# Optimization experiments

Hardware: AMD Instinct MI355X
Metric: run time of the kernel (lower is better)

## Reference

```python
import jax, jax.numpy as jnp
import numpy as np

N = 100000   # nodes
E = 3200000  # edges (before self-loops)
IN, H, OUT = 128, 256, 40

def glorot(key, shape):
    lim = (6.0 / (shape[0] + shape[1])) ** 0.5
    return jax.random.uniform(key, shape, jnp.float32, -lim, lim)

def setup_inputs() -> dict:
    key = jax.random.key(0)
    ks = jax.random.split(key, 8)
    x = jax.random.normal(ks[0], (N, IN), jnp.float32)
    edge_index = jax.random.randint(ks[1], (2, E), 0, N, dtype=jnp.int32)
    return {
        "x": x,
        "edge_index": edge_index,
        "W0": glorot(ks[2], (IN, H)),  "b0": jnp.zeros((H,), jnp.float32),
        "W1": glorot(ks[3], (H, H)),   "b1": jnp.zeros((H,), jnp.float32),
        "W2": glorot(ks[4], (H, OUT)), "b2": jnp.zeros((OUT,), jnp.float32),
    }

def _gcn_norm(edge_index, n):
    # PyG gcn_norm: add self-loops, symmetric D^{-1/2} A D^{-1/2}
    loops = jnp.arange(n, dtype=edge_index.dtype)
    src = jnp.concatenate([edge_index[0], loops])
    dst = jnp.concatenate([edge_index[1], loops])
    deg = jax.ops.segment_sum(jnp.ones_like(src, jnp.float32), dst, num_segments=n)
    dinv = jnp.where(deg > 0, jax.lax.rsqrt(deg), 0.0)
    norm = dinv[src] * dinv[dst]  # [E+N]
    return src, dst, norm

def _gcn_layer(h, W, b, src, dst, norm, n):
    h = h @ W                                   # transform first (PyG order)
    msg = h[src] * norm[:, None]                # gather + scale
    agg = jax.ops.segment_sum(msg, dst, num_segments=n)  # scatter-add
    return agg + b

def reference(x, edge_index, W0, b0, W1, b1, W2, b2):
    n = x.shape[0]
    src, dst, norm = _gcn_norm(edge_index, n)
    h = jnp.tanh(_gcn_layer(x, W0, b0, src, dst, norm, n))  # dropout = identity (eval)
    h = jnp.tanh(_gcn_layer(h, W1, b1, src, dst, norm, n))
    out = _gcn_layer(h, W2, b2, src, dst, norm, n)
    return jax.nn.log_softmax(out, axis=1)
```

## Files before the change

### kernel.cpp

```cpp
#include <hip/hip_runtime.h>
#include <hip/hip_bf16.h>
#include <cmath>


typedef unsigned short u16;
typedef __attribute__((ext_vector_type(8))) short short8;
typedef __attribute__((ext_vector_type(4))) float f32x4;

#define BSHIFT 10
#define BNODES (1 << BSHIFT)
#define ECAP   36864
#define BMASK 0x00FF00FFu

__device__ __forceinline__ u16 f2bf(float f) {
    unsigned int u = __float_as_uint(f);
    u += 0x7fffu + ((u >> 16) & 1u);
    return (u16)(u >> 16);
}
__device__ __forceinline__ float bflo(unsigned int u) { return __uint_as_float(u << 16); }
__device__ __forceinline__ float bfhi(unsigned int u) { return __uint_as_float(u & 0xffff0000u); }

__device__ __forceinline__ int q8(float v) {
    return (int)rintf(fminf(fmaxf(v, -127.0f), 127.0f));
}


__global__ __launch_bounds__(128) void init_gcur_kernel(
        int* __restrict__ gcur, int nb) {
    int b = blockIdx.x * 128 + threadIdx.x;
    if (b < nb) gcur[b] = b * ECAP;
}

__global__ __launch_bounds__(256) void bucketize_kernel(
        const int* __restrict__ src, const int* __restrict__ dst,
        int* __restrict__ gcur, unsigned int* __restrict__ ebuf, int E) {
    __shared__ int cnt[128];
    __shared__ int base[128];
    int tid = threadIdx.x;
    int chunk0 = blockIdx.x * 8192;
    int cend = min(chunk0 + 8192, E);
    for (int r0 = chunk0; r0 < cend; r0 += 2048) {
        if (tid < 128) cnt[tid] = 0;
        __syncthreads();
        int rank[8], bk[8];
        unsigned int pk[8];
#pragma unroll
        for (int j = 0; j < 8; j++) {
            int e = r0 + j * 256 + tid;
            bk[j] = -1;
            if (e < cend) {
                int d = dst[e];
                bk[j] = d >> BSHIFT;
                pk[j] = (unsigned int)src[e] | ((unsigned int)(d & (BNODES - 1)) << 17);
                rank[j] = atomicAdd(&cnt[bk[j]], 1);
            }
        }
        __syncthreads();
        if (tid < 128 && cnt[tid] > 0) base[tid] = atomicAdd(&gcur[tid], cnt[tid]);
        __syncthreads();
#pragma unroll
        for (int j = 0; j < 8; j++)
            if (bk[j] >= 0) ebuf[base[bk[j]] + rank[j]] = pk[j];
        __syncthreads();
    }
}

__global__ __launch_bounds__(256) void deg_hist_kernel(
        const unsigned int* __restrict__ ebuf, const int* __restrict__ gcur,
        int* __restrict__ degi, int N) {
    __shared__ int h[BNODES];
    int b = blockIdx.x;
    int nb0 = b << BSHIFT;
    int nodes = min(BNODES, N - nb0);
    for (int i = threadIdx.x; i < nodes; i += 256) h[i] = 0;
    __syncthreads();
    int estart = b * ECAP;
    int eend = gcur[b];
    for (int e = estart + threadIdx.x; e < eend; e += 256)
        atomicAdd(&h[ebuf[e] >> 17], 1);
    __syncthreads();
    for (int i = threadIdx.x; i < nodes; i += 256) degi[nb0 + i] = h[i];
}

__global__ __launch_bounds__(256) void dinv_kernel(
        const int* __restrict__ degi, float* __restrict__ dinv, int n) {
    int i = blockIdx.x * 256 + threadIdx.x;
    if (i < n) dinv[i] = rsqrtf((float)degi[i] + 1.0f);
}

__global__ __launch_bounds__(256) void scan_part_kernel(
        const int* __restrict__ deg, int* __restrict__ part, int n) {
    __shared__ int s[256];
    int i = blockIdx.x * 256 + threadIdx.x;
    s[threadIdx.x] = (i < n) ? deg[i] : 0;
    __syncthreads();
    for (int off = 128; off; off >>= 1) {
        if (threadIdx.x < off) s[threadIdx.x] += s[threadIdx.x + off];
        __syncthreads();
    }
    if (threadIdx.x == 0) part[blockIdx.x] = s[0];
}

__global__ __launch_bounds__(1024) void scan_top_kernel(
        int* __restrict__ part, int nb) {
    __shared__ int s[1024];
    int t = threadIdx.x;
    int v = (t < nb) ? part[t] : 0;
    s[t] = v;
    __syncthreads();
    for (int off = 1; off < 1024; off <<= 1) {
        int u = (t >= off) ? s[t - off] : 0;
        __syncthreads();
        s[t] += u;
        __syncthreads();
    }
    if (t < nb) part[t] = s[t] - v;
}

__global__ __launch_bounds__(256) void scan_apply_kernel(
        const int* __restrict__ deg, const int* __restrict__ part,
        int* __restrict__ rs, int n) {
    __shared__ int s[256];
    int i = blockIdx.x * 256 + threadIdx.x;
    int v = (i < n) ? deg[i] : 0;
    s[threadIdx.x] = v;
    __syncthreads();
    for (int off = 1; off < 256; off <<= 1) {
        int u = (threadIdx.x >= off) ? s[threadIdx.x - off] : 0;
        __syncthreads();
        s[threadIdx.x] += u;
        __syncthreads();
    }
    if (i < n) rs[i] = part[blockIdx.x] + s[threadIdx.x] - v;
}

__global__ __launch_bounds__(256) void csr_fill_kernel(
        const unsigned int* __restrict__ ebuf, const int* __restrict__ gcur,
        const int* __restrict__ rs, int* __restrict__ csr, int N) {
    __shared__ int lcur[BNODES];
    int b = blockIdx.x;
    int nb0 = b << BSHIFT;
    int nodes = min(BNODES, N - nb0);
    for (int i = threadIdx.x; i < nodes; i += 256) lcur[i] = rs[nb0 + i];
    __syncthreads();
    int estart = b * ECAP;
    int eend = gcur[b];
    for (int e = estart + threadIdx.x; e < eend; e += 256) {
        unsigned int v = ebuf[e];
        int s = v & 0x1FFFF;
        int dl = v >> 17;
        int pos = atomicAdd(&lcur[dl], 1);
        csr[pos] = s;
    }
}

__global__ __launch_bounds__(256) void wt_kernel(
        const float* __restrict__ W, u16* __restrict__ Wt, int K, int NC) {
    int i = blockIdx.x * 256 + threadIdx.x;
    if (i < K * NC) {
        int k = i / NC, c = i % NC;
        Wt[(size_t)c * K + k] = f2bf(W[i]);
    }
}

__global__ __launch_bounds__(256) void scale_x_kernel(
        const float* __restrict__ x, const float* __restrict__ dinv,
        unsigned int* __restrict__ out, int total4) {
    int i = blockIdx.x * 256 + threadIdx.x;
    if (i >= total4) return;
    int n = i >> 5;
    float4 v = reinterpret_cast<const float4*>(x)[i];
    float s = dinv[n] * 63.5f;
    int a0 = q8(v.x * s), a1 = q8(v.y * s), a2 = q8(v.z * s), a3 = q8(v.w * s);
    out[i] = (unsigned int)(a0 & 0xff) | ((unsigned int)(a1 & 0xff) << 8) |
             ((unsigned int)(a2 & 0xff) << 16) | ((unsigned int)(a3 & 0xff) << 24);
}

#define ACC8(q0, q1)                                                  \
    do {                                                              \
        aex += (q0) & BMASK; aox += ((q0) >> 8) & BMASK;              \
        aey += (q1) & BMASK; aoy += ((q1) >> 8) & BMASK;              \
    } while (0)

__global__ __launch_bounds__(256) void agg128_i8_kernel(
        const signed char* __restrict__ in, u16* __restrict__ out,
        const int* __restrict__ rs, const int* __restrict__ deg,
        const int* __restrict__ csr, const float* __restrict__ dinv, int n) {
    int wid = blockIdx.x * 4 + (threadIdx.x >> 6);
    if (wid >= n) return;
    int lane = threadIdx.x & 63;
    int quad = lane >> 4;
    int l16 = lane & 15;
    int start = rs[wid];
    int cnt = deg[wid];

    unsigned int aex = 0, aox = 0, aey = 0, aoy = 0;
    if (quad == 0) {
        uint2 q = *reinterpret_cast<const uint2*>(
            in + (size_t)wid * 128 + l16 * 8);
        q.x ^= 0x80808080u; q.y ^= 0x80808080u;
        ACC8(q.x, q.y);
    }
    int i = 0;
    for (; i + 16 <= cnt; i += 16) {
        int s[4];
#pragma unroll
        for (int j = 0; j < 4; j++) s[j] = csr[start + i + 4 * j + quad];
#pragma unroll
        for (int j = 0; j < 4; j++) {
            uint2 q = *reinterpret_cast<const uint2*>(
                in + (size_t)s[j] * 128 + l16 * 8);
            q.x ^= 0x80808080u; q.y ^= 0x80808080u;
            ACC8(q.x, q.y);
        }
    }
    for (; i + 4 <= cnt; i += 4) {
        int s0 = csr[start + i + quad];
        uint2 q = *reinterpret_cast<const uint2*>(
            in + (size_t)s0 * 128 + l16 * 8);
        q.x ^= 0x80808080u; q.y ^= 0x80808080u;
        ACC8(q.x, q.y);
    }
    int rem = cnt - i;
    if (quad < rem) {
        int s0 = csr[start + i + quad];
        uint2 q = *reinterpret_cast<const uint2*>(
            in + (size_t)s0 * 128 + l16 * 8);
        q.x ^= 0x80808080u; q.y ^= 0x80808080u;
        ACC8(q.x, q.y);
    }
    aex += (unsigned int)__shfl((int)aex, lane + 32);
    aox += (unsigned int)__shfl((int)aox, lane + 32);
    aey += (unsigned int)__shfl((int)aey, lane + 32);
    aoy += (unsigned int)__shfl((int)aoy, lane + 32);
    aex += (unsigned int)__shfl((int)aex, lane + 16);
    aox += (unsigned int)__shfl((int)aox, lane + 16);
    aey += (unsigned int)__shfl((int)aey, lane + 16);
    aoy += (unsigned int)__shfl((int)aoy, lane + 16);
    if (lane < 16) {
        int T = cnt + 1;
        int bias = 128 * T;
        float c = dinv[wid] * (2.0f / 127.0f);
        float f0 = (float)((int)(aex & 0xFFFFu) - bias) * c;
        float f1 = (float)((int)(aox & 0xFFFFu) - bias) * c;
        float f2 = (float)((int)(aex >> 16) - bias) * c;
        float f3 = (float)((int)(aox >> 16) - bias) * c;
        float f4 = (float)((int)(aey & 0xFFFFu) - bias) * c;
        float f5 = (float)((int)(aoy & 0xFFFFu) - bias) * c;
        float f6 = (float)((int)(aey >> 16) - bias) * c;
        float f7 = (float)((int)(aoy >> 16) - bias) * c;
        uint4 o;
        o.x = (unsigned)f2bf(f0) | ((unsigned)f2bf(f1) << 16);
        o.y = (unsigned)f2bf(f2) | ((unsigned)f2bf(f3) << 16);
        o.z = (unsigned)f2bf(f4) | ((unsigned)f2bf(f5) << 16);
        o.w = (unsigned)f2bf(f6) | ((unsigned)f2bf(f7) << 16);
        reinterpret_cast<uint4*>(out + (size_t)wid * 128)[l16] = o;
    }
}

__global__ __launch_bounds__(256) void agg_i8_kernel(
        const signed char* __restrict__ in, u16* __restrict__ out,
        const int* __restrict__ rs, const int* __restrict__ deg,
        const int* __restrict__ csr, const float* __restrict__ dinv, int n) {
    int wid = blockIdx.x * 4 + (threadIdx.x >> 6);
    if (wid >= n) return;
    int lane = threadIdx.x & 63;
    int start = rs[wid];
    int cnt = deg[wid];

    unsigned int q = *reinterpret_cast<const unsigned int*>(
        in + (size_t)wid * 256 + lane * 4) ^ 0x80808080u;
    unsigned int ae = q & BMASK, ao = (q >> 8) & BMASK;

    int i = 0;
    for (; i + 16 <= cnt; i += 16) {
        int s[16];
#pragma unroll
        for (int j = 0; j < 16; j++)
            s[j] = __builtin_amdgcn_readfirstlane(csr[start + i + j]);
        unsigned int qq[16];
#pragma unroll
        for (int j = 0; j < 16; j++)
            qq[j] = *reinterpret_cast<const unsigned int*>(
                in + (size_t)s[j] * 256 + lane * 4);
#pragma unroll
        for (int j = 0; j < 16; j++) {
            unsigned int v = qq[j] ^ 0x80808080u;
            ae += v & BMASK;
            ao += (v >> 8) & BMASK;
        }
    }
    if (i < cnt) {
        int s[16];
#pragma unroll
        for (int j = 0; j < 16; j++) {
            int e = i + j;
            e = (e < cnt) ? e : (cnt - 1);
            s[j] = __builtin_amdgcn_readfirstlane(csr[start + e]);
        }
        unsigned int qq[16];
#pragma unroll
        for (int j = 0; j < 16; j++)
            qq[j] = *reinterpret_cast<const unsigned int*>(
                in + (size_t)s[j] * 256 + lane * 4);
#pragma unroll
        for (int j = 0; j < 16; j++) {
            unsigned int m = (i + j < cnt) ? 0xFFFFFFFFu : 0u;
            unsigned int v = (qq[j] ^ 0x80808080u) & m;
            ae += v & BMASK;
            ao += (v >> 8) & BMASK;
        }
    }

    int bias = 128 * (cnt + 1);
    float c = dinv[wid] * (1.0f / 127.0f);
    float f0 = (float)((int)(ae & 0xFFFFu) - bias) * c;
    float f1 = (float)((int)(ao & 0xFFFFu) - bias) * c;
    float f2 = (float)((int)(ae >> 16) - bias) * c;
    float f3 = (float)((int)(ao >> 16) - bias) * c;
    uint2 o;
    o.x = (unsigned)f2bf(f0) | ((unsigned)f2bf(f1) << 16);
    o.y = (unsigned)f2bf(f2) | ((unsigned)f2bf(f3) << 16);
    reinterpret_cast<uint2*>(out + (size_t)wid * 256)[lane] = o;
}

template<int EPI, typename CT>
__global__ __launch_bounds__(256) void mfma_mm_kernel(
        const u16* __restrict__ A, const u16* __restrict__ Bt,
        CT* __restrict__ C, int M, int K, int NC,
        const float* __restrict__ bias, const float* __restrict__ postscale,
        float qs) {
    __shared__ u16 As[128 * 40];
    __shared__ u16 Bs[64 * 40];
    int t = threadIdx.x;
    int w = t >> 6, lane = t & 63, quad = lane >> 4, l16 = lane & 15;
    int row0 = blockIdx.x * 128;
    int col0 = blockIdx.y * 64;

    f32x4 acc[2][4];
#pragma unroll
    for (int s = 0; s < 2; s++)
#pragma unroll
        for (int nb = 0; nb < 4; nb++)
            acc[s][nb] = (f32x4){0.f, 0.f, 0.f, 0.f};

    int bn = t >> 2, bkq = (t & 3) << 3;
    for (int k0 = 0; k0 < K; k0 += 32) {
#pragma unroll
        for (int i = t; i < 512; i += 256) {
            int r = i >> 2, c = (i & 3) << 3;
            int gr = row0 + r;
            uint4 v = {0u, 0u, 0u, 0u};
            if (gr < M)
                v = *reinterpret_cast<const uint4*>(A + (size_t)gr * K + k0 + c);
            *reinterpret_cast<uint4*>(&As[r * 40 + c]) = v;
        }
        {
            int gc = col0 + bn;
            uint4 v = {0u, 0u, 0u, 0u};
            if (gc < NC)
                v = *reinterpret_cast<const uint4*>(Bt + (size_t)gc * K + k0 + bkq);
            *reinterpret_cast<uint4*>(&Bs[bn * 40 + bkq]) = v;
        }
        __syncthreads();

        short8 af[2], bf[4];
        af[0] = *reinterpret_cast<const short8*>(&As[(w * 32 + l16) * 40 + quad * 8]);
        af[1] = *reinterpret_cast<const short8*>(&As[(w * 32 + 16 + l16) * 40 + quad * 8]);
#pragma unroll
        for (int nb = 0; nb < 4; nb++)
            bf[nb] = *reinterpret_cast<const short8*>(&Bs[(nb * 16 + l16) * 40 + quad * 8]);
#pragma unroll
        for (int s = 0; s < 2; s++)
#pragma unroll
            for (int nb = 0; nb < 4; nb++)
                acc[s][nb] = __builtin_amdgcn_mfma_f32_16x16x32_bf16(
                    af[s], bf[nb], acc[s][nb], 0, 0, 0);
        __syncthreads();
    }

#pragma unroll
    for (int s = 0; s < 2; s++) {
        int rbase = row0 + w * 32 + s * 16 + quad * 4;
#pragma unroll
        for (int nb = 0; nb < 4; nb++) {
            int gc = col0 + nb * 16 + l16;
#pragma unroll
            for (int r = 0; r < 4; r++) {
                int gr = rbase + r;
                if (gr >= M || gc >= NC) continue;
                float v = acc[s][nb][r];
                if constexpr (EPI == 1) v = tanhf(v + bias[gc]);
                else                    v = v * postscale[gr];
                if constexpr (sizeof(CT) == 1) {
                    float m = qs;
                    if constexpr (EPI == 1) m *= postscale[gr];
                    C[(size_t)gr * NC + gc] = (CT)q8(v * m);
                } else {
                    C[(size_t)gr * NC + gc] = (CT)f2bf(v);
                }
            }
        }
    }
}

__global__ __launch_bounds__(256) void agg40_ls_kernel(
        const signed char* __restrict__ in, const int* __restrict__ rs,
        const int* __restrict__ deg, const int* __restrict__ csr,
        const float* __restrict__ dinv, const float* __restrict__ bias,
        float* __restrict__ out, int n) {
    int wid = blockIdx.x * 4 + (threadIdx.x >> 6);
    if (wid >= n) return;
    int lane = threadIdx.x & 63;
    int grp = lane / 5;
    int l5 = lane - grp * 5;
    bool act = lane < 60;
    int start = rs[wid];
    int cnt = deg[wid];

    unsigned int aex = 0, aox = 0, aey = 0, aoy = 0;
    if (lane < 5) {
        uint2 q = *reinterpret_cast<const uint2*>(
            in + (size_t)wid * 40 + l5 * 8);
        q.x ^= 0x80808080u; q.y ^= 0x80808080u;
        ACC8(q.x, q.y);
    }
    for (int base = 0; base < cnt; base += 12) {
        int e = base + grp;
        if (act && e < cnt) {
            int s0 = csr[start + e];
            uint2 q = *reinterpret_cast<const uint2*>(
                in + (size_t)s0 * 40 + l5 * 8);
            q.x ^= 0x80808080u; q.y ^= 0x80808080u;
            ACC8(q.x, q.y);
        }
    }
    aex += (unsigned int)__shfl((int)aex, lane + 30);
    aox += (unsigned int)__shfl((int)aox, lane + 30);
    aey += (unsigned int)__shfl((int)aey, lane + 30);
    aoy += (unsigned int)__shfl((int)aoy, lane + 30);
    aex += (unsigned int)__shfl((int)aex, lane + 15);
    aox += (unsigned int)__shfl((int)aox, lane + 15);
    aey += (unsigned int)__shfl((int)aey, lane + 15);
    aoy += (unsigned int)__shfl((int)aoy, lane + 15);
    aex += (unsigned int)__shfl((int)aex, lane + 5) + (unsigned int)__shfl((int)aex, lane + 10);
    aox += (unsigned int)__shfl((int)aox, lane + 5) + (unsigned int)__shfl((int)aox, lane + 10);
    aey += (unsigned int)__shfl((int)aey, lane + 5) + (unsigned int)__shfl((int)aey, lane + 10);
    aoy += (unsigned int)__shfl((int)aoy, lane + 5) + (unsigned int)__shfl((int)aoy, lane + 10);

    bool act5 = lane < 5;
    float s = dinv[wid];
    float v0 = -INFINITY, v1 = -INFINITY, v2 = -INFINITY, v3 = -INFINITY;
    float v4 = -INFINITY, v5 = -INFINITY, v6 = -INFINITY, v7 = -INFINITY;
    if (act5) {
        int bb = 128 * (cnt + 1);
        float c = s * (1.0f / 63.0f);
        int cc = lane * 8;
        v0 = (float)((int)(aex & 0xFFFFu) - bb) * c + bias[cc + 0];
        v1 = (float)((int)(aox & 0xFFFFu) - bb) * c + bias[cc + 1];
        v2 = (float)((int)(aex >> 16) - bb) * c + bias[cc + 2];
        v3 = (float)((int)(aox >> 16) - bb) * c + bias[cc + 3];
        v4 = (float)((int)(aey & 0xFFFFu) - bb) * c + bias[cc + 4];
        v5 = (float)((int)(aoy & 0xFFFFu) - bb) * c + bias[cc + 5];
        v6 = (float)((int)(aey >> 16) - bb) * c + bias[cc + 6];
        v7 = (float)((int)(aoy >> 16) - bb) * c + bias[cc + 7];
    }
    float m = fmaxf(fmaxf(fmaxf(v0, v1), fmaxf(v2, v3)),
                    fmaxf(fmaxf(v4, v5), fmaxf(v6, v7)));
    for (int off = 4; off; off >>= 1) m = fmaxf(m, __shfl_xor(m, off));
    float e = 0.f;
    if (act5) e = __expf(v0 - m) + __expf(v1 - m) + __expf(v2 - m) + __expf(v3 - m)
                + __expf(v4 - m) + __expf(v5 - m) + __expf(v6 - m) + __expf(v7 - m);
    for (int off = 4; off; off >>= 1) e += __shfl_xor(e, off);
    float ls = logf(e);
    if (act5) {
        float4 o0, o1;
        o0.x = v0 - m - ls; o0.y = v1 - m - ls; o0.z = v2 - m - ls; o0.w = v3 - m - ls;
        o1.x = v4 - m - ls; o1.y = v5 - m - ls; o1.z = v6 - m - ls; o1.w = v7 - m - ls;
        float4* op = reinterpret_cast<float4*>(out + (size_t)wid * 40 + lane * 8);
        op[0] = o0;
        op[1] = o1;
    }
}

extern "C" void kernel_launch(void* const* d_in, const int* in_sizes, int n_in,
                              void* d_out, int out_size, void* d_ws, size_t ws_size,
                              hipStream_t stream) {
    const float* x  = (const float*)d_in[0];
    const int*   ei = (const int*)d_in[1];
    const float* W0 = (const float*)d_in[2];
    const float* b0 = (const float*)d_in[3];
    const float* W1 = (const float*)d_in[4];
    const float* b1 = (const float*)d_in[5];
    const float* W2 = (const float*)d_in[6];
    const float* b2 = (const float*)d_in[7];
    float* out = (float*)d_out;

    const int N = in_sizes[0] / 128;
    const int E = in_sizes[1] / 2;
    const int IN = 128, H = 256, OUT = 40;
    const int NB = (N + BNODES - 1) >> BSHIFT;

    char* p = (char*)d_ws;
    auto carve = [&](size_t bytes) -> void* {
        void* r = (void*)p;
        p += (bytes + 255) & ~(size_t)255;
        return r;
    };
    float*        dinv = (float*)carve((size_t)N * 4);
    int*          degi = (int*)  carve((size_t)N * 4);
    int*          rs   = (int*)  carve((size_t)N * 4);
    int*          part = (int*)  carve((size_t)1024 * 4);
    int*          gcur = (int*)  carve((size_t)128 * 4);
    int*          csr  = (int*)  carve((size_t)E * 4);
    unsigned int* ebuf = (unsigned int*)carve((size_t)NB * ECAP * 4);
    u16*          Wt0  = (u16*)  carve((size_t)IN * H * 2);
    u16*          Wt1  = (u16*)  carve((size_t)H * H * 2);
    u16*          Wt2  = (u16*)  carve((size_t)H * OUT * 2);
    u16*          U1   = (u16*)  carve((size_t)N * H * 2);
    u16*          U2   = (u16*)  carve((size_t)N * H * 2);

    signed char* Xq   = (signed char*)U1;
    u16*         T0bf = U1 + (size_t)N * IN / 2 + 64;
    signed char* H0q  = (signed char*)U2;
    u16*         T1bf = U1;
    u16*         h1bf = U2;
    signed char* G2q  = (signed char*)U1;

    const int* src = ei;
    const int* dst = ei + E;

    int gN = (N + 255) / 256;
    int gW = (N + 3) / 4;
    int gMM = (N + 127) / 128;
    int gA = (E + 8191) / 8192;

    init_gcur_kernel<<<1, 128, 0, stream>>>(gcur, NB);
    bucketize_kernel<<<gA, 256, 0, stream>>>(src, dst, gcur, ebuf, E);
    deg_hist_kernel<<<NB, 256, 0, stream>>>(ebuf, gcur, degi, N);
    dinv_kernel<<<gN, 256, 0, stream>>>(degi, dinv, N);
    scan_part_kernel<<<gN, 256, 0, stream>>>(degi, part, N);
    scan_top_kernel<<<1, 1024, 0, stream>>>(part, gN);
    scan_apply_kernel<<<gN, 256, 0, stream>>>(degi, part, rs, N);
    csr_fill_kernel<<<NB, 256, 0, stream>>>(ebuf, gcur, rs, csr, N);

    wt_kernel<<<(IN * H + 255) / 256, 256, 0, stream>>>(W0, Wt0, IN, H);
    wt_kernel<<<(H * H + 255) / 256, 256, 0, stream>>>(W1, Wt1, H, H);
    wt_kernel<<<(H * OUT + 255) / 256, 256, 0, stream>>>(W2, Wt2, H, OUT);

    int t4x = N * (IN / 4);
    scale_x_kernel<<<(t4x + 255) / 256, 256, 0, stream>>>(
        x, dinv, (unsigned int*)Xq, t4x);
    agg128_i8_kernel<<<gW, 256, 0, stream>>>(Xq, T0bf, rs, degi, csr, dinv, N);
    mfma_mm_kernel<1, signed char><<<dim3(gMM, H / 64), 256, 0, stream>>>(
        T0bf, Wt0, H0q, N, IN, H, b0, dinv, 127.0f);

    agg_i8_kernel<<<gW, 256, 0, stream>>>(H0q, T1bf, rs, degi, csr, dinv, N);
    mfma_mm_kernel<1, u16><<<dim3(gMM, H / 64), 256, 0, stream>>>(
        T1bf, Wt1, h1bf, N, H, H, b1, nullptr, 0.f);

    mfma_mm_kernel<0, signed char><<<dim3(gMM, 1), 256, 0, stream>>>(
        h1bf, Wt2, G2q, N, H, OUT, nullptr, dinv, 63.0f);
    agg40_ls_kernel<<<gW, 256, 0, stream>>>(G2q, rs, degi, csr, dinv, b2, out, N);
}
```

Baseline: 625.2 us.

## Fuse dinv into degree histogram, merge weight transposes, widen GEMM column tiles

Computes dinv inside deg_hist_kernel and merges the three weight-transpose launches into one, which removes kernel launches. The MFMA GEMM is templated on the number of 16-column blocks. The two 256-wide layers now use 128-column tiles, halving re-reads of A. The 40-column final layer uses 3 blocks instead of 4, which cuts wasted MFMA work on padding. Wider tiles use more accumulator registers and halve the grid size for the hidden layers.

```diff
diff --git a/kernel.cpp b/kernel.cpp
--- a/kernel.cpp
+++ b/kernel.cpp
@@ -17,8 +17,6 @@
     u += 0x7fffu + ((u >> 16) & 1u);
     return (u16)(u >> 16);
 }
-__device__ __forceinline__ float bflo(unsigned int u) { return __uint_as_float(u << 16); }
-__device__ __forceinline__ float bfhi(unsigned int u) { return __uint_as_float(u & 0xffff0000u); }
 
 __device__ __forceinline__ int q8(float v) {
     return (int)rintf(fminf(fmaxf(v, -127.0f), 127.0f));
@@ -67,7 +65,7 @@
 
 __global__ __launch_bounds__(256) void deg_hist_kernel(
         const unsigned int* __restrict__ ebuf, const int* __restrict__ gcur,
-        int* __restrict__ degi, int N) {
+        int* __restrict__ degi, float* __restrict__ dinv, int N) {
     __shared__ int h[BNODES];
     int b = blockIdx.x;
     int nb0 = b << BSHIFT;
@@ -79,13 +77,11 @@
     for (int e = estart + threadIdx.x; e < eend; e += 256)
         atomicAdd(&h[ebuf[e] >> 17], 1);
     __syncthreads();
-    for (int i = threadIdx.x; i < nodes; i += 256) degi[nb0 + i] = h[i];
-}
-
-__global__ __launch_bounds__(256) void dinv_kernel(
-        const int* __restrict__ degi, float* __restrict__ dinv, int n) {
-    int i = blockIdx.x * 256 + threadIdx.x;
-    if (i < n) dinv[i] = rsqrtf((float)degi[i] + 1.0f);
+    for (int i = threadIdx.x; i < nodes; i += 256) {
+        int d = h[i];
+        degi[nb0 + i] = d;
+        dinv[nb0 + i] = rsqrtf((float)d + 1.0f);
+    }
 }
 
 __global__ __launch_bounds__(256) void scan_part_kernel(
@@ -154,12 +150,22 @@
     }
 }
 
-__global__ __launch_bounds__(256) void wt_kernel(
-        const float* __restrict__ W, u16* __restrict__ Wt, int K, int NC) {
+__global__ __launch_bounds__(256) void wt_all_kernel(
+        const float* __restrict__ W0, const float* __restrict__ W1,
+        const float* __restrict__ W2, u16* __restrict__ Wt0,
+        u16* __restrict__ Wt1, u16* __restrict__ Wt2) {
     int i = blockIdx.x * 256 + threadIdx.x;
-    if (i < K * NC) {
-        int k = i / NC, c = i % NC;
-        Wt[(size_t)c * K + k] = f2bf(W[i]);
+    if (i < 32768) {
+        int k = i >> 8, c = i & 255;
+        Wt0[c * 128 + k] = f2bf(W0[i]);
+    } else if (i < 98304) {
+        int j = i - 32768;
+        int k = j >> 8, c = j & 255;
+        Wt1[c * 256 + k] = f2bf(W1[j]);
+    } else if (i < 108544) {
+        int j = i - 98304;
+        int k = j / 40, c = j - k * 40;
+        Wt2[c * 256 + k] = f2bf(W2[j]);
     }
 }
 
@@ -324,27 +330,26 @@
     reinterpret_cast<uint2*>(out + (size_t)wid * 256)[lane] = o;
 }
 
-template<int EPI, typename CT>
+template<int EPI, typename CT, int NCB>
 __global__ __launch_bounds__(256) void mfma_mm_kernel(
         const u16* __restrict__ A, const u16* __restrict__ Bt,
         CT* __restrict__ C, int M, int K, int NC,
         const float* __restrict__ bias, const float* __restrict__ postscale,
         float qs) {
     __shared__ u16 As[128 * 40];
-    __shared__ u16 Bs[64 * 40];
+    __shared__ u16 Bs[NCB * 16 * 40];
     int t = threadIdx.x;
     int w = t >> 6, lane = t & 63, quad = lane >> 4, l16 = lane & 15;
     int row0 = blockIdx.x * 128;
-    int col0 = blockIdx.y * 64;
-
-    f32x4 acc[2][4];
+    int col0 = blockIdx.y * (NCB * 16);
+
+    f32x4 acc[2][NCB];
 #pragma unroll
     for (int s = 0; s < 2; s++)
 #pragma unroll
-        for (int nb = 0; nb < 4; nb++)
+        for (int nb = 0; nb < NCB; nb++)
             acc[s][nb] = (f32x4){0.f, 0.f, 0.f, 0.f};
 
-    int bn = t >> 2, bkq = (t & 3) << 3;
     for (int k0 = 0; k0 < K; k0 += 32) {
 #pragma unroll
         for (int i = t; i < 512; i += 256) {
@@ -355,27 +360,27 @@
                 v = *reinterpret_cast<const uint4*>(A + (size_t)gr * K + k0 + c);
             *reinterpret_cast<uint4*>(&As[r * 40 + c]) = v;
         }
-        {
-            int gc = col0 + bn;
+#pragma unroll
+        for (int i = t; i < NCB * 64; i += 256) {
+            int c = i >> 2, kq = (i & 3) << 3;
+            int gc = col0 + c;
             uint4 v = {0u, 0u, 0u, 0u};
             if (gc < NC)
-                v = *reinterpret_cast<const uint4*>(Bt + (size_t)gc * K + k0 + bkq);
-            *reinterpret_cast<uint4*>(&Bs[bn * 40 + bkq]) = v;
-        }
-        __syncthreads();
-
-        short8 af[2], bf[4];
+                v = *reinterpret_cast<const uint4*>(Bt + (size_t)gc * K + k0 + kq);
+            *reinterpret_cast<uint4*>(&Bs[c * 40 + kq]) = v;
+        }
+        __syncthreads();
+
+        short8 af[2];
         af[0] = *reinterpret_cast<const short8*>(&As[(w * 32 + l16) * 40 + quad * 8]);
         af[1] = *reinterpret_cast<const short8*>(&As[(w * 32 + 16 + l16) * 40 + quad * 8]);
 #pragma unroll
-        for (int nb = 0; nb < 4; nb++)
-            bf[nb] = *reinterpret_cast<const short8*>(&Bs[(nb * 16 + l16) * 40 + quad * 8]);
-#pragma unroll
-        for (int s = 0; s < 2; s++)
-#pragma unroll
-            for (int nb = 0; nb < 4; nb++)
-                acc[s][nb] = __builtin_amdgcn_mfma_f32_16x16x32_bf16(
-                    af[s], bf[nb], acc[s][nb], 0, 0, 0);
+        for (int nb = 0; nb < NCB; nb++) {
+            short8 bf = *reinterpret_cast<const short8*>(
+                &Bs[(nb * 16 + l16) * 40 + quad * 8]);
+            acc[0][nb] = __builtin_amdgcn_mfma_f32_16x16x32_bf16(af[0], bf, acc[0][nb], 0, 0, 0);
+            acc[1][nb] = __builtin_amdgcn_mfma_f32_16x16x32_bf16(af[1], bf, acc[1][nb], 0, 0, 0);
+        }
         __syncthreads();
     }
 
@@ -383,7 +388,7 @@
     for (int s = 0; s < 2; s++) {
         int rbase = row0 + w * 32 + s * 16 + quad * 4;
 #pragma unroll
-        for (int nb = 0; nb < 4; nb++) {
+        for (int nb = 0; nb < NCB; nb++) {
             int gc = col0 + nb * 16 + l16;
 #pragma unroll
             for (int r = 0; r < 4; r++) {
@@ -537,29 +542,27 @@
 
     init_gcur_kernel<<<1, 128, 0, stream>>>(gcur, NB);
     bucketize_kernel<<<gA, 256, 0, stream>>>(src, dst, gcur, ebuf, E);
-    deg_hist_kernel<<<NB, 256, 0, stream>>>(ebuf, gcur, degi, N);
-    dinv_kernel<<<gN, 256, 0, stream>>>(degi, dinv, N);
+    deg_hist_kernel<<<NB, 256, 0, stream>>>(ebuf, gcur, degi, dinv, N);
     scan_part_kernel<<<gN, 256, 0, stream>>>(degi, part, N);
     scan_top_kernel<<<1, 1024, 0, stream>>>(part, gN);
     scan_apply_kernel<<<gN, 256, 0, stream>>>(degi, part, rs, N);
     csr_fill_kernel<<<NB, 256, 0, stream>>>(ebuf, gcur, rs, csr, N);
 
-    wt_kernel<<<(IN * H + 255) / 256, 256, 0, stream>>>(W0, Wt0, IN, H);
-    wt_kernel<<<(H * H + 255) / 256, 256, 0, stream>>>(W1, Wt1, H, H);
-    wt_kernel<<<(H * OUT + 255) / 256, 256, 0, stream>>>(W2, Wt2, H, OUT);
+    wt_all_kernel<<<(108544 + 255) / 256, 256, 0, stream>>>(
+        W0, W1, W2, Wt0, Wt1, Wt2);
 
     int t4x = N * (IN / 4);
     scale_x_kernel<<<(t4x + 255) / 256, 256, 0, stream>>>(
         x, dinv, (unsigned int*)Xq, t4x);
     agg128_i8_kernel<<<gW, 256, 0, stream>>>(Xq, T0bf, rs, degi, csr, dinv, N);
-    mfma_mm_kernel<1, signed char><<<dim3(gMM, H / 64), 256, 0, stream>>>(
+    mfma_mm_kernel<1, signed char, 8><<<dim3(gMM, H / 128), 256, 0, stream>>>(
         T0bf, Wt0, H0q, N, IN, H, b0, dinv, 127.0f);
 
     agg_i8_kernel<<<gW, 256, 0, stream>>>(H0q, T1bf, rs, degi, csr, dinv, N);
-    mfma_mm_kernel<1, u16><<<dim3(gMM, H / 64), 256, 0, stream>>>(
+    mfma_mm_kernel<1, u16, 8><<<dim3(gMM, H / 128), 256, 0, stream>>>(
         T1bf, Wt1, h1bf, N, H, H, b1, nullptr, 0.f);
 
-    mfma_mm_kernel<0, signed char><<<dim3(gMM, 1), 256, 0, stream>>>(
+    mfma_mm_kernel<0, signed char, 3><<<dim3(gMM, 1), 256, 0, stream>>>(
         h1bf, Wt2, G2q, N, H, OUT, nullptr, dinv, 63.0f);
     agg40_ls_kernel<<<gW, 256, 0, stream>>>(G2q, rs, degi, csr, dinv, b2, out, N);
 }
```

Result: slower. 668.2 us (+6.9%).
